# Kernel tuning notes

Measured on AMD Instinct MI355X. Metric: run time of the kernel, lower is better.

Reference implementation:

```python
import jax, jax.numpy as jnp
import numpy as np

NUM_ANGLE = 100
NUM_RHO = 100
EPS = 1e-5


def _dht_rho_indices(h, w, num_angle, num_rho):
    # Per the deep-hough-transform CUDA host code:
    # irho = (floor(sqrt(H^2+W^2)) + 1) / (numRho - 1); theta_k = k*pi/numAngle
    irho = (int(np.sqrt(h * h + w * w)) + 1) / float(num_rho - 1)
    theta = np.arange(num_angle) * (np.pi / num_angle)
    cos_t = np.cos(theta) / irho  # [A]
    sin_t = np.sin(theta) / irho
    yy = (np.arange(h) - h // 2).astype(np.float64)  # centered row coord
    xx = (np.arange(w) - w // 2).astype(np.float64)  # centered col coord
    # r[a, i, j] = round(xx*cos + yy*sin) + numRho//2
    r = np.round(xx[None, None, :] * cos_t[:, None, None]
                 + yy[None, :, None] * sin_t[:, None, None]).astype(np.int32)
    r = np.clip(r + num_rho // 2, 0, num_rho - 1)
    return jnp.asarray(r.reshape(num_angle, h * w))  # [A, HW]


def dht(feat, num_angle, num_rho):
    # Hough voting: scatter-add every pixel into one rho bin per angle.
    n, c, h, w = feat.shape
    idx = _dht_rho_indices(h, w, num_angle, num_rho)      # [A, HW] int32
    flat = feat.reshape(n * c, h * w).T                   # [HW, NC]
    seg = lambda ids: jax.ops.segment_sum(flat, ids, num_segments=num_rho)
    acc = jax.vmap(seg)(idx)                              # [A, R, NC]
    return acc.transpose(2, 0, 1).reshape(n, c, num_angle, num_rho)


def conv2d(x, wgt, b, pad):
    y = jax.lax.conv_general_dilated(
        x, wgt, window_strides=(1, 1), padding=[(pad, pad), (pad, pad)],
        dimension_numbers=("NCHW", "OIHW", "NCHW"))
    return y + b[None, :, None, None]


def bn_relu(x, gamma, beta):
    # BatchNorm in eval mode with running_mean=0, running_var=1.
    scale = gamma / np.sqrt(1.0 + EPS)
    return jax.nn.relu(x * scale[None, :, None, None] + beta[None, :, None, None])


def setup_inputs() -> dict:
    key = jax.random.key(0)
    ks = jax.random.split(key, 4)
    N, CIN, DIM, H, W = 16, 256, 128, 100, 100
    x = jax.random.normal(ks[0], (N, CIN, H, W), dtype=jnp.float32)
    w1 = jax.random.normal(ks[1], (DIM, CIN, 1, 1), dtype=jnp.float32) * 0.05
    w2 = jax.random.normal(ks[2], (DIM, DIM, 3, 3), dtype=jnp.float32) * 0.05
    w3 = jax.random.normal(ks[3], (DIM, DIM, 3, 3), dtype=jnp.float32) * 0.05
    zeros = jnp.zeros((DIM,), jnp.float32)
    ones = jnp.ones((DIM,), jnp.float32)
    return {
        "x": x,
        "w1": w1, "b1": zeros, "g1": ones, "be1": zeros,
        "w2": w2, "b2": zeros, "g2": ones, "be2": zeros,
        "w3": w3, "b3": zeros, "g3": ones, "be3": zeros,
    }


def reference(x, w1, b1, g1, be1, w2, b2, g2, be2, w3, b3, g3, be3):
    h = bn_relu(conv2d(x, w1, b1, 0), g1, be1)        # 1x1 conv + BN + ReLU
    h = dht(h, NUM_ANGLE, NUM_RHO)                    # Hough voting -> [N,C,A,R]
    h = bn_relu(conv2d(h, w2, b2, 1), g2, be2)        # 3x3 conv + BN + ReLU
    h = bn_relu(conv2d(h, w3, b3, 1), g3, be3)        # 3x3 conv + BN + ReLU
    return h
```

## Files before the change

### kernel.cpp

```cpp
#include <hip/hip_runtime.h>
#include <hip/hip_bf16.h>
#include <math.h>

#ifndef M_PI
#define M_PI 3.14159265358979323846
#endif

typedef unsigned short u16;
typedef short short8 __attribute__((ext_vector_type(8)));
typedef float f32x4 __attribute__((ext_vector_type(4)));
typedef float f32x2 __attribute__((ext_vector_type(2)));

#define CIN  256
#define CH   128
#define HW   10000
#define NA   100
#define NR   100

__device__ __forceinline__ float bf2f(u16 v) {
  return __uint_as_float(((unsigned int)v) << 16);
}
__device__ __forceinline__ u16 f2bf(float f) {
  unsigned int u = __float_as_uint(f);
  u += 0x7fffu + ((u >> 16) & 1u);
  return (u16)(u >> 16);
}
__device__ __forceinline__ f32x2 bfpair(unsigned int v) {
  f32x2 r;
  r.x = __uint_as_float(v << 16);
  r.y = __uint_as_float(v & 0xffff0000u);
  return r;
}

__global__ void __launch_bounds__(256)
k_prep_csr(const float* __restrict__ w1, const float* __restrict__ w2,
           const float* __restrict__ w3, u16* __restrict__ wbf1,
           u16* __restrict__ wbf2, u16* __restrict__ wbf3,
           u16* __restrict__ list, int* __restrict__ coff,
           int* __restrict__ woff) {
#pragma clang fp contract(off)
  __shared__ unsigned char sidx[HW];
  __shared__ unsigned short rowcnt[100][100];
  __shared__ int off[NR + 1];
  __shared__ int wstart[17];
  int b = blockIdx.x;
  int t = threadIdx.x;

  if (b >= 100) {
    int tt = (b - 100) * 256 + t;
    if (tt < 32768) {
      int j = tt & 7, lp = (tt >> 3) & 63, nf = (tt >> 9) & 7, kc = tt >> 12;
      int co = nf * 16 + (lp & 15);
      int ci = kc * 32 + (lp >> 4) * 8 + j;
      wbf1[tt] = f2bf(w1[co * CIN + ci]);
    }
    {
      int j = tt & 7, lp = (tt >> 3) & 63, nf = (tt >> 9) & 7, kc = (tt >> 12) & 3, tap = tt >> 14;
      int co = nf * 16 + (lp & 15);
      int ci = kc * 32 + (lp >> 4) * 8 + j;
      wbf2[tt] = f2bf(w2[(co * CH + ci) * 9 + tap]);
      wbf3[tt] = f2bf(w3[(co * CH + ci) * 9 + tap]);
    }
    return;
  }

  int a = b;
  double theta = (double)a * (M_PI / 100.0);
  double irho  = 142.0 / 99.0;
  double ct = cos(theta) / irho;
  double st = sin(theta) / irho;

  if (t < 100) {
    for (int q = 0; q < 50; ++q) ((unsigned int*)&rowcnt[t][0])[q] = 0;
    int base = t * 100;
    for (int j = 0; j < 100; ++j) {
      double s = (double)(j - 50) * ct + (double)(t - 50) * st;
      int r = (int)rint(s) + 50;
      r = r < 0 ? 0 : (r > 99 ? 99 : r);
      sidx[base + j] = (unsigned char)r;
      rowcnt[t][r]++;
    }
  }
  if (t < 17) wstart[t] = NR;
  __syncthreads();

  if (t < 100) {
    int running = 0;
    for (int cc = 0; cc < 100; ++cc) {
      int tmp = rowcnt[cc][t];
      rowcnt[cc][t] = (unsigned short)running;
      running += tmp;
    }
    off[t + 1] = running;
  }
  __syncthreads();

  if (t == 0) {
    off[0] = 0;
    for (int bb = 0; bb < NR; ++bb) {
      int cb = off[bb + 1];
      off[bb + 1] = off[bb] + cb;
    }
  }
  __syncthreads();
  if (t <= NR) coff[a * (NR + 1) + t] = off[t];

  if (t < NR) {
    int o0 = off[t], o1 = off[t + 1];
    int ow = (o0 + ((o1 - o0) >> 1)) * 16 / HW;
    ow = ow > 15 ? 15 : ow;
    atomicMin(&wstart[ow], t);
  }
  __syncthreads();
  if (t == 0) {
    wstart[16] = NR;
    for (int ww = 15; ww >= 0; --ww)
      if (wstart[ww] == NR) wstart[ww] = wstart[ww + 1];
  }
  __syncthreads();
  if (t < 17) woff[a * 20 + t] = wstart[t];

  if (t < 100) {
    u16* dst = list + (size_t)a * HW;
    int base = t * 100;
    for (int j = 0; j < 100; ++j) {
      int r = sidx[base + j];
      int pos = off[r] + rowcnt[t][r];
      rowcnt[t][r]++;
      dst[pos] = (u16)(base + j);
    }
  }
}

__global__ void __launch_bounds__(256)
k_xt(const float* __restrict__ x, u16* __restrict__ xt) {
  __shared__ u16 tl[64][70];
  int n = blockIdx.z, c0 = blockIdx.y * 64, h0 = blockIdx.x * 64;
  int t = threadIdx.x;
#pragma unroll
  for (int p = 0; p < 16; ++p) {
    int row = p * 4 + (t >> 6);
    int col = t & 63;
    int hw  = h0 + col;
    float v = (hw < HW) ? x[((size_t)n * CIN + c0 + row) * HW + hw] : 0.f;
    tl[row][col] = f2bf(v);
  }
  __syncthreads();
  int hr = t >> 2;
  int sc = (t & 3) * 16;
  int hw = h0 + hr;
  if (hw < HW) {
    u16 vals[16];
#pragma unroll
    for (int j = 0; j < 16; ++j) vals[j] = tl[sc + j][hr];
    u16* dst = xt + ((size_t)n * HW + hw) * CIN + c0 + sc;
    *(uint4*)(dst)     = *(uint4*)&vals[0];
    *(uint4*)(dst + 8) = *(uint4*)&vals[8];
  }
}

__global__ void __launch_bounds__(512)
k_conv1(const u16* __restrict__ xt, const u16* __restrict__ wbf1,
        const float* __restrict__ pb, const float* __restrict__ pg,
        const float* __restrict__ pbe, u16* __restrict__ h1t) {
  __shared__ uint4 lds4[4096];
  char* lds = (char*)lds4;
  int n  = blockIdx.y;
  int m0 = blockIdx.x * 128;
  int t  = threadIdx.x;
  int l  = t & 63, w = t >> 6, wm = w >> 2, wn = w & 3;

  {
    int r16 = t >> 5;
    int seg = t & 31;
#pragma unroll
    for (int p = 0; p < 8; ++p) {
      int m  = p * 16 + r16;
      int hw = m0 + m;
      uint4 v = make_uint4(0, 0, 0, 0);
      if (hw < HW) v = *(const uint4*)(xt + ((size_t)n * HW + hw) * CIN + seg * 8);
      *(uint4*)(lds + m * 512 + ((seg * 16) ^ ((m & 31) << 4))) = v;
    }
  }
  __syncthreads();

  int kseg = (l >> 4) * 16;
  f32x4 acc[4][2];
  f32x4 zf = {0.f, 0.f, 0.f, 0.f};
#pragma unroll
  for (int i = 0; i < 4; ++i)
#pragma unroll
    for (int j = 0; j < 2; ++j) acc[i][j] = zf;

  for (int kc = 0; kc < 8; ++kc) {
    short8 afr[4], bfr[2];
#pragma unroll
    for (int fm = 0; fm < 4; ++fm) {
      int m = wm * 64 + fm * 16 + (l & 15);
      afr[fm] = *(const short8*)(lds + m * 512 + ((kc * 64 + kseg) ^ ((m & 31) << 4)));
    }
#pragma unroll
    for (int fn = 0; fn < 2; ++fn)
      bfr[fn] = *(const short8*)(wbf1 + (((size_t)kc * 8 + wn * 2 + fn) * 64 + l) * 8);
#pragma unroll
    for (int fm = 0; fm < 4; ++fm)
#pragma unroll
      for (int fn = 0; fn < 2; ++fn)
        acc[fm][fn] = __builtin_amdgcn_mfma_f32_16x16x32_bf16(afr[fm], bfr[fn], acc[fm][fn], 0, 0, 0);
  }

  float sc[2], sh[2];
#pragma unroll
  for (int fn = 0; fn < 2; ++fn) {
    int co = wn * 32 + fn * 16 + (l & 15);
    float s = pg[co] / sqrtf(1.f + 1e-5f);
    sc[fn] = s;
    sh[fn] = pb[co] * s + pbe[co];
  }

  __syncthreads();
#pragma unroll
  for (int fm = 0; fm < 4; ++fm)
#pragma unroll
    for (int fn = 0; fn < 2; ++fn) {
      int co = wn * 32 + fn * 16 + (l & 15);
#pragma unroll
      for (int q = 0; q < 4; ++q) {
        int m = wm * 64 + fm * 16 + (l >> 4) * 4 + q;
        float y = fmaxf(acc[fm][fn][q] * sc[fn] + sh[fn], 0.f);
        *(u16*)(lds + m * 256 + ((co * 2) ^ ((m & 15) << 4))) = f2bf(y);
      }
    }
  __syncthreads();
#pragma unroll
  for (int p = 0; p < 4; ++p) {
    int e = p * 512 + t;
    int m = e >> 4;
    int hw = m0 + m;
    if (hw < HW) {
      uint4 v = *(const uint4*)(lds + m * 256 + (((e & 15) * 16) ^ ((m & 15) << 4)));
      *(uint4*)(h1t + ((size_t)n * HW + hw) * CH + (e & 15) * 8) = v;
    }
  }
}

__global__ void __launch_bounds__(256)
k_dht(const u16* __restrict__ h1t, const u16* __restrict__ list,
      const int* __restrict__ coff, const int* __restrict__ woff,
      u16* __restrict__ dht) {
  int id  = blockIdx.x;
  int x   = id & 7;
  int rem = id >> 3;
  int hi  = rem >= 400;
  int n   = (x << 1) | hi;
  int aq  = hi ? rem - 400 : rem;
  int a   = aq >> 2;
  int q   = aq & 3;
  int t   = threadIdx.x;
  int c   = t & 63;
  int w   = (t >> 6) + q * 4;

  const char* nimg = (const char*)h1t + (size_t)n * HW * 256;
  const int  c4    = c * 4;
  const u16* lst   = list + (size_t)a * HW;
  const int* cof   = coff + a * (NR + 1);
  const int* wof   = woff + a * 20;
  unsigned int* out32 = (unsigned int*)(dht + ((size_t)(n * NA + a) * NR) * CH) + c;

  int rlo = __builtin_amdgcn_readfirstlane(wof[w]);
  int rhi = __builtin_amdgcn_readfirstlane(wof[w + 1]);
  if (rlo >= rhi) return;

  int o0 = __builtin_amdgcn_readfirstlane(cof[rlo]);
  for (int r = rlo; r < rhi; ++r) {
    int o1 = __builtin_amdgcn_readfirstlane(cof[r + 1]);

    f32x2 A0 = {0.f, 0.f}, A1 = {0.f, 0.f};
    int k = o0;

    if (k & 1) {
      int p = __builtin_amdgcn_readfirstlane((int)lst[k]);
      unsigned int v = *(const unsigned int*)((nimg + ((size_t)p << 8)) + c4);
      A0 += bfpair(v);
      ++k;
    }

    for (; k + 16 <= o1; k += 16) {
      unsigned int ids[8];
#pragma unroll
      for (int j = 0; j < 8; ++j)
        ids[j] = __builtin_amdgcn_readfirstlane(*(const unsigned int*)(lst + k + 2 * j));
      unsigned int v[16];
#pragma unroll
      for (int j = 0; j < 8; ++j) {
        int p0 = (int)(ids[j] & 0xffffu);
        int p1 = (int)(ids[j] >> 16);
        v[2 * j]     = *(const unsigned int*)((nimg + ((size_t)p0 << 8)) + c4);
        v[2 * j + 1] = *(const unsigned int*)((nimg + ((size_t)p1 << 8)) + c4);
      }
#pragma unroll
      for (int j = 0; j < 16; ++j) {
        if (j & 1) A1 += bfpair(v[j]);
        else       A0 += bfpair(v[j]);
      }
    }
    for (; k + 2 <= o1; k += 2) {
      unsigned int ids = __builtin_amdgcn_readfirstlane(*(const unsigned int*)(lst + k));
      int p0 = (int)(ids & 0xffffu);
      int p1 = (int)(ids >> 16);
      unsigned int v0 = *(const unsigned int*)((nimg + ((size_t)p0 << 8)) + c4);
      unsigned int v1 = *(const unsigned int*)((nimg + ((size_t)p1 << 8)) + c4);
      A0 += bfpair(v0);
      A1 += bfpair(v1);
    }
    if (k < o1) {
      int p = __builtin_amdgcn_readfirstlane((int)lst[k]);
      unsigned int v = *(const unsigned int*)((nimg + ((size_t)p << 8)) + c4);
      A0 += bfpair(v);
    }

    float ax = A0.x + A1.x;
    float ay = A0.y + A1.y;
    unsigned int pk = (unsigned int)f2bf(ax) | ((unsigned int)f2bf(ay) << 16);
    out32[(size_t)r << 6] = pk;
    o0 = o1;
  }
}

template <int OUT_MODE>
__global__ void __launch_bounds__(512)
k_conv3x3(const u16* __restrict__ X, const u16* __restrict__ wbf,
          const float* __restrict__ pb, const float* __restrict__ pg,
          const float* __restrict__ pbe, void* __restrict__ out) {
  __shared__ uint4 lds4[2880];
  char* lds = (char*)lds4;
  int n    = blockIdx.y;
  int tile = blockIdx.x;
  int ta = tile / 13, tr = tile - ta * 13;
  int a0 = ta * 16, r0 = tr * 8;
  int t  = threadIdx.x;
  int l  = t & 63, w = t >> 6, wm = w >> 2, wn = w & 3;

  {
    int sr32 = t >> 4;
    int cb   = (t & 15) * 16;
#pragma unroll
    for (int p = 0; p < 6; ++p) {
      int s = p * 32 + sr32;
      if (s < 180) {
        int sa = a0 - 1 + s / 10;
        int sr = r0 - 1 + s % 10;
        uint4 v = make_uint4(0, 0, 0, 0);
        if (sa >= 0 && sa < NA && sr >= 0 && sr < NR)
          v = *(const uint4*)(X + ((size_t)(n * NA + sa) * NR + sr) * CH + (t & 15) * 8);
        *(uint4*)(lds + s * 256 + (cb ^ ((s & 15) << 4))) = v;
      }
    }
  }
  __syncthreads();

  int sbase[4];
#pragma unroll
  for (int fm = 0; fm < 4; ++fm) {
    int m = wm * 64 + fm * 16 + (l & 15);
    sbase[fm] = ((m >> 3) + 1) * 10 + (m & 7) + 1;
  }
  int kseg = (l >> 4) * 16;

  f32x4 acc[4][2];
  f32x4 zf = {0.f, 0.f, 0.f, 0.f};
#pragma unroll
  for (int i = 0; i < 4; ++i)
#pragma unroll
    for (int j = 0; j < 2; ++j) acc[i][j] = zf;

  for (int tap = 0; tap < 9; ++tap) {
    int soff = (tap / 3 - 1) * 10 + (tap % 3 - 1);
#pragma unroll
    for (int kc = 0; kc < 4; ++kc) {
      short8 afr[4], bfr[2];
#pragma unroll
      for (int fm = 0; fm < 4; ++fm) {
        int s = sbase[fm] + soff;
        afr[fm] = *(const short8*)(lds + s * 256 + ((kc * 64 + kseg) ^ ((s & 15) << 4)));
      }
#pragma unroll
      for (int fn = 0; fn < 2; ++fn)
        bfr[fn] = *(const short8*)(wbf + (((size_t)(tap * 4 + kc) * 8 + wn * 2 + fn) * 64 + l) * 8);
#pragma unroll
      for (int fm = 0; fm < 4; ++fm)
#pragma unroll
        for (int fn = 0; fn < 2; ++fn)
          acc[fm][fn] = __builtin_amdgcn_mfma_f32_16x16x32_bf16(afr[fm], bfr[fn], acc[fm][fn], 0, 0, 0);
    }
  }

  float sc[2], sh[2];
#pragma unroll
  for (int fn = 0; fn < 2; ++fn) {
    int co = wn * 32 + fn * 16 + (l & 15);
    float s = pg[co] / sqrtf(1.f + 1e-5f);
    sc[fn] = s;
    sh[fn] = pb[co] * s + pbe[co];
  }

  if (OUT_MODE == 0) {
    __syncthreads();
#pragma unroll
    for (int fm = 0; fm < 4; ++fm)
#pragma unroll
      for (int fn = 0; fn < 2; ++fn) {
        int co = wn * 32 + fn * 16 + (l & 15);
#pragma unroll
        for (int q = 0; q < 4; ++q) {
          int m = wm * 64 + fm * 16 + (l >> 4) * 4 + q;
          float y = fmaxf(acc[fm][fn][q] * sc[fn] + sh[fn], 0.f);
          *(u16*)(lds + m * 256 + ((co * 2) ^ ((m & 15) << 4))) = f2bf(y);
        }
      }
    __syncthreads();
    u16* o = (u16*)out;
#pragma unroll
    for (int p = 0; p < 4; ++p) {
      int e = p * 512 + t;
      int m = e >> 4;
      int a = a0 + (m >> 3), r = r0 + (m & 7);
      if (a < NA && r < NR) {
        uint4 v = *(const uint4*)(lds + m * 256 + (((e & 15) * 16) ^ ((m & 15) << 4)));
        *(uint4*)(o + ((size_t)(n * NA + a) * NR + r) * CH + (e & 15) * 8) = v;
      }
    }
  } else {
    float* o = (float*)out;
#pragma unroll
    for (int fm = 0; fm < 4; ++fm) {
      int mb = wm * 64 + fm * 16 + (l >> 4) * 4;
      int a  = a0 + (mb >> 3), rr = r0 + (mb & 7);
      if (a < NA && rr < NR) {
#pragma unroll
        for (int fn = 0; fn < 2; ++fn) {
          int co = wn * 32 + fn * 16 + (l & 15);
          float4 v;
          v.x = fmaxf(acc[fm][fn][0] * sc[fn] + sh[fn], 0.f);
          v.y = fmaxf(acc[fm][fn][1] * sc[fn] + sh[fn], 0.f);
          v.z = fmaxf(acc[fm][fn][2] * sc[fn] + sh[fn], 0.f);
          v.w = fmaxf(acc[fm][fn][3] * sc[fn] + sh[fn], 0.f);
          *(float4*)(o + ((size_t)n * CH + co) * HW + a * NR + rr) = v;
        }
      }
    }
  }
}

extern "C" void kernel_launch(void* const* d_in, const int* in_sizes, int n_in,
                              void* d_out, int out_size, void* d_ws, size_t ws_size,
                              hipStream_t stream) {
  if (n_in < 13) return;
  const float* x   = (const float*)d_in[0];
  const float* w1  = (const float*)d_in[1];
  const float* b1  = (const float*)d_in[2];
  const float* g1  = (const float*)d_in[3];
  const float* be1 = (const float*)d_in[4];
  const float* w2  = (const float*)d_in[5];
  const float* b2  = (const float*)d_in[6];
  const float* g2  = (const float*)d_in[7];
  const float* be2 = (const float*)d_in[8];
  const float* w3  = (const float*)d_in[9];
  const float* b3  = (const float*)d_in[10];
  const float* g3  = (const float*)d_in[11];
  const float* be3 = (const float*)d_in[12];

  const size_t o_list = 0;
  const size_t o_coff = 2000128;
  const size_t o_woff = 2040576;
  const size_t o_wbf1 = 2048768;
  const size_t o_wbf2 = o_wbf1 + 65536;
  const size_t o_wbf3 = o_wbf2 + 294912;
  const size_t o_dht  = o_wbf3 + 294912;
  const size_t o_c2   = o_dht + 40960000;
  const size_t need   = o_dht + 81920000;
  if (ws_size < need) return;

  char*  ws   = (char*)d_ws;
  u16*   list = (u16*)(ws + o_list);
  int*   coff = (int*)(ws + o_coff);
  int*   woff = (int*)(ws + o_woff);
  u16*   wbf1 = (u16*)(ws + o_wbf1);
  u16*   wbf2 = (u16*)(ws + o_wbf2);
  u16*   wbf3 = (u16*)(ws + o_wbf3);
  u16*   xt   = (u16*)(ws + o_dht);
  u16*   dht  = (u16*)(ws + o_dht);
  u16*   c2   = (u16*)(ws + o_c2);
  u16*   h1t  = (u16*)d_out;

  k_prep_csr<<<dim3(676), dim3(256), 0, stream>>>(w1, w2, w3, wbf1, wbf2, wbf3, list, coff, woff);
  k_xt<<<dim3(157, 4, 16), dim3(256), 0, stream>>>(x, xt);
  k_conv1<<<dim3(79, 16), dim3(512), 0, stream>>>(xt, wbf1, b1, g1, be1, h1t);
  k_dht<<<dim3(6400), dim3(256), 0, stream>>>(h1t, list, coff, woff, dht);
  k_conv3x3<0><<<dim3(91, 16), dim3(512), 0, stream>>>(dht, wbf2, b2, g2, be2, (void*)c2);
  k_conv3x3<1><<<dim3(91, 16), dim3(512), 0, stream>>>(c2, wbf3, b3, g3, be3, d_out);
}
```

Before: 415.5 us.

## Switch 3x3 conv MFMA from 16x16x32 to 32x32x16 with new warp tiling

Rewrites the 3x3 conv inner loop to use 32x32x16 bf16 MFMA instructions, with each wave covering 32 rows by 64 output channels instead of 64 by 32. The conv2/conv3 weight pre-pack layout is changed to match the new B-fragment layout, and both epilogues are remapped to the 32x32 accumulator register layout. The aim is fewer MFMA issues and fewer LDS A-fragment reads per FLOP. In exchange, B-fragment global loads per wave double relative to A reuse.

```diff
diff --git a/kernel.cpp b/kernel.cpp
--- a/kernel.cpp
+++ b/kernel.cpp
@@ -10,6 +10,7 @@
 typedef short short8 __attribute__((ext_vector_type(8)));
 typedef float f32x4 __attribute__((ext_vector_type(4)));
 typedef float f32x2 __attribute__((ext_vector_type(2)));
+typedef float f32x16 __attribute__((ext_vector_type(16)));
 
 #define CIN  256
 #define CH   128
@@ -55,9 +56,13 @@
       wbf1[tt] = f2bf(w1[co * CIN + ci]);
     }
     {
-      int j = tt & 7, lp = (tt >> 3) & 63, nf = (tt >> 9) & 7, kc = (tt >> 12) & 3, tap = tt >> 14;
-      int co = nf * 16 + (lp & 15);
-      int ci = kc * 32 + (lp >> 4) * 8 + j;
+      int j   = tt & 7;
+      int lp  = (tt >> 3) & 63;
+      int nf  = (tt >> 9) & 3;
+      int k16 = (tt >> 11) & 7;
+      int tap = tt >> 14;
+      int co  = nf * 32 + (lp & 31);
+      int ci  = k16 * 16 + (lp >> 5) * 8 + j;
       wbf2[tt] = f2bf(w2[(co * CH + ci) * 9 + tap]);
       wbf3[tt] = f2bf(w3[(co * CH + ci) * 9 + tap]);
     }
@@ -339,7 +344,7 @@
   int ta = tile / 13, tr = tile - ta * 13;
   int a0 = ta * 16, r0 = tr * 8;
   int t  = threadIdx.x;
-  int l  = t & 63, w = t >> 6, wm = w >> 2, wn = w & 3;
+  int l  = t & 63, w = t >> 6, wm = w >> 1, wn = w & 1;
 
   {
     int sr32 = t >> 4;
@@ -359,46 +364,37 @@
   }
   __syncthreads();
 
-  int sbase[4];
-#pragma unroll
-  for (int fm = 0; fm < 4; ++fm) {
-    int m = wm * 64 + fm * 16 + (l & 15);
-    sbase[fm] = ((m >> 3) + 1) * 10 + (m & 7) + 1;
-  }
-  int kseg = (l >> 4) * 16;
-
-  f32x4 acc[4][2];
-  f32x4 zf = {0.f, 0.f, 0.f, 0.f};
-#pragma unroll
-  for (int i = 0; i < 4; ++i)
-#pragma unroll
-    for (int j = 0; j < 2; ++j) acc[i][j] = zf;
+  int mrow  = wm * 32 + (l & 31);
+  int sbase = ((mrow >> 3) + 1) * 10 + (mrow & 7) + 1;
+  int kcol  = (l >> 5) * 16;
+
+  f32x16 acc[2];
+#pragma unroll
+  for (int i = 0; i < 2; ++i)
+#pragma unroll
+    for (int q = 0; q < 16; ++q) acc[i][q] = 0.f;
 
   for (int tap = 0; tap < 9; ++tap) {
     int soff = (tap / 3 - 1) * 10 + (tap % 3 - 1);
-#pragma unroll
-    for (int kc = 0; kc < 4; ++kc) {
-      short8 afr[4], bfr[2];
-#pragma unroll
-      for (int fm = 0; fm < 4; ++fm) {
-        int s = sbase[fm] + soff;
-        afr[fm] = *(const short8*)(lds + s * 256 + ((kc * 64 + kseg) ^ ((s & 15) << 4)));
-      }
+    int s = sbase + soff;
+    int sw = (s & 15) << 4;
+#pragma unroll
+    for (int k16 = 0; k16 < 8; ++k16) {
+      short8 afr = *(const short8*)(lds + s * 256 + ((k16 * 32 + kcol) ^ sw));
+      short8 bfr[2];
 #pragma unroll
       for (int fn = 0; fn < 2; ++fn)
-        bfr[fn] = *(const short8*)(wbf + (((size_t)(tap * 4 + kc) * 8 + wn * 2 + fn) * 64 + l) * 8);
-#pragma unroll
-      for (int fm = 0; fm < 4; ++fm)
-#pragma unroll
-        for (int fn = 0; fn < 2; ++fn)
-          acc[fm][fn] = __builtin_amdgcn_mfma_f32_16x16x32_bf16(afr[fm], bfr[fn], acc[fm][fn], 0, 0, 0);
+        bfr[fn] = *(const short8*)(wbf + (((size_t)(tap * 8 + k16) * 4 + wn * 2 + fn) * 64 + l) * 8);
+#pragma unroll
+      for (int fn = 0; fn < 2; ++fn)
+        acc[fn] = __builtin_amdgcn_mfma_f32_32x32x16_bf16(afr, bfr[fn], acc[fn], 0, 0, 0);
     }
   }
 
   float sc[2], sh[2];
 #pragma unroll
   for (int fn = 0; fn < 2; ++fn) {
-    int co = wn * 32 + fn * 16 + (l & 15);
+    int co = wn * 64 + fn * 32 + (l & 31);
     float s = pg[co] / sqrtf(1.f + 1e-5f);
     sc[fn] = s;
     sh[fn] = pb[co] * s + pbe[co];
@@ -407,17 +403,15 @@
   if (OUT_MODE == 0) {
     __syncthreads();
 #pragma unroll
-    for (int fm = 0; fm < 4; ++fm)
-#pragma unroll
-      for (int fn = 0; fn < 2; ++fn) {
-        int co = wn * 32 + fn * 16 + (l & 15);
-#pragma unroll
-        for (int q = 0; q < 4; ++q) {
-          int m = wm * 64 + fm * 16 + (l >> 4) * 4 + q;
-          float y = fmaxf(acc[fm][fn][q] * sc[fn] + sh[fn], 0.f);
-          *(u16*)(lds + m * 256 + ((co * 2) ^ ((m & 15) << 4))) = f2bf(y);
-        }
-      }
+    for (int fn = 0; fn < 2; ++fn) {
+      int co = wn * 64 + fn * 32 + (l & 31);
+#pragma unroll
+      for (int reg = 0; reg < 16; ++reg) {
+        int m = wm * 32 + (reg & 3) + 8 * (reg >> 2) + 4 * (l >> 5);
+        float y = fmaxf(acc[fn][reg] * sc[fn] + sh[fn], 0.f);
+        *(u16*)(lds + m * 256 + ((co * 2) ^ ((m & 15) << 4))) = f2bf(y);
+      }
+    }
     __syncthreads();
     u16* o = (u16*)out;
 #pragma unroll
@@ -433,18 +427,18 @@
   } else {
     float* o = (float*)out;
 #pragma unroll
-    for (int fm = 0; fm < 4; ++fm) {
-      int mb = wm * 64 + fm * 16 + (l >> 4) * 4;
-      int a  = a0 + (mb >> 3), rr = r0 + (mb & 7);
-      if (a < NA && rr < NR) {
-#pragma unroll
-        for (int fn = 0; fn < 2; ++fn) {
-          int co = wn * 32 + fn * 16 + (l & 15);
+    for (int fn = 0; fn < 2; ++fn) {
+      int co = wn * 64 + fn * 32 + (l & 31);
+#pragma unroll
+      for (int q = 0; q < 4; ++q) {
+        int mb = wm * 32 + 8 * q + 4 * (l >> 5);
+        int a  = a0 + (mb >> 3), rr = r0 + (mb & 7);
+        if (a < NA && rr < NR) {
           float4 v;
-          v.x = fmaxf(acc[fm][fn][0] * sc[fn] + sh[fn], 0.f);
-          v.y = fmaxf(acc[fm][fn][1] * sc[fn] + sh[fn], 0.f);
-          v.z = fmaxf(acc[fm][fn][2] * sc[fn] + sh[fn], 0.f);
-          v.w = fmaxf(acc[fm][fn][3] * sc[fn] + sh[fn], 0.f);
+          v.x = fmaxf(acc[fn][4 * q + 0] * sc[fn] + sh[fn], 0.f);
+          v.y = fmaxf(acc[fn][4 * q + 1] * sc[fn] + sh[fn], 0.f);
+          v.z = fmaxf(acc[fn][4 * q + 2] * sc[fn] + sh[fn], 0.f);
+          v.w = fmaxf(acc[fn][4 * q + 3] * sc[fn] + sh[fn], 0.f);
           *(float4*)(o + ((size_t)n * CH + co) * HW + a * NR + rr) = v;
         }
       }
```

New measurement: 446.7 us. 1.08x slower.

## Fuse input transpose into 1x1 conv and fold BN scale into weights

Applied to the files above, without the earlier changes.

Removes the separate transpose/bf16-cast kernel. The 1x1 conv now reads fp32 NCHW input directly and converts it to bf16 in registers, with weights as the A operand and pixels as the B operand. The BN scale is folded into the bf16 weights during prep, and a precomputed bias vector replaces the per-thread scale/shift math. This saves one full write and read of the transposed activation, but the input loads are now strided per channel (8 separate loads per fragment) rather than vectorized 16-byte loads.

```diff
diff --git a/kernel.cpp b/kernel.cpp
--- a/kernel.cpp
+++ b/kernel.cpp
@@ -34,8 +34,10 @@
 
 __global__ void __launch_bounds__(256)
 k_prep_csr(const float* __restrict__ w1, const float* __restrict__ w2,
-           const float* __restrict__ w3, u16* __restrict__ wbf1,
-           u16* __restrict__ wbf2, u16* __restrict__ wbf3,
+           const float* __restrict__ w3, const float* __restrict__ g1,
+           const float* __restrict__ b1, const float* __restrict__ be1,
+           u16* __restrict__ wbf1, u16* __restrict__ wbf2,
+           u16* __restrict__ wbf3, float* __restrict__ bias1,
            u16* __restrict__ list, int* __restrict__ coff,
            int* __restrict__ woff) {
 #pragma clang fp contract(off)
@@ -52,7 +54,12 @@
       int j = tt & 7, lp = (tt >> 3) & 63, nf = (tt >> 9) & 7, kc = tt >> 12;
       int co = nf * 16 + (lp & 15);
       int ci = kc * 32 + (lp >> 4) * 8 + j;
-      wbf1[tt] = f2bf(w1[co * CIN + ci]);
+      float s = g1[co] / sqrtf(1.f + 1e-5f);
+      wbf1[tt] = f2bf(w1[co * CIN + ci] * s);
+    }
+    if (b == 100 && t < 128) {
+      float s = g1[t] / sqrtf(1.f + 1e-5f);
+      bias1[t] = b1[t] * s + be1[t];
     }
     {
       int j = tt & 7, lp = (tt >> 3) & 63, nf = (tt >> 9) & 7, kc = (tt >> 12) & 3, tap = tt >> 14;
@@ -132,59 +139,19 @@
   }
 }
 
-__global__ void __launch_bounds__(256)
-k_xt(const float* __restrict__ x, u16* __restrict__ xt) {
-  __shared__ u16 tl[64][70];
-  int n = blockIdx.z, c0 = blockIdx.y * 64, h0 = blockIdx.x * 64;
-  int t = threadIdx.x;
-#pragma unroll
-  for (int p = 0; p < 16; ++p) {
-    int row = p * 4 + (t >> 6);
-    int col = t & 63;
-    int hw  = h0 + col;
-    float v = (hw < HW) ? x[((size_t)n * CIN + c0 + row) * HW + hw] : 0.f;
-    tl[row][col] = f2bf(v);
-  }
-  __syncthreads();
-  int hr = t >> 2;
-  int sc = (t & 3) * 16;
-  int hw = h0 + hr;
-  if (hw < HW) {
-    u16 vals[16];
-#pragma unroll
-    for (int j = 0; j < 16; ++j) vals[j] = tl[sc + j][hr];
-    u16* dst = xt + ((size_t)n * HW + hw) * CIN + c0 + sc;
-    *(uint4*)(dst)     = *(uint4*)&vals[0];
-    *(uint4*)(dst + 8) = *(uint4*)&vals[8];
-  }
-}
-
 __global__ void __launch_bounds__(512)
-k_conv1(const u16* __restrict__ xt, const u16* __restrict__ wbf1,
-        const float* __restrict__ pb, const float* __restrict__ pg,
-        const float* __restrict__ pbe, u16* __restrict__ h1t) {
-  __shared__ uint4 lds4[4096];
-  char* lds = (char*)lds4;
-  int n  = blockIdx.y;
-  int m0 = blockIdx.x * 128;
-  int t  = threadIdx.x;
-  int l  = t & 63, w = t >> 6, wm = w >> 2, wn = w & 3;
-
-  {
-    int r16 = t >> 5;
-    int seg = t & 31;
-#pragma unroll
-    for (int p = 0; p < 8; ++p) {
-      int m  = p * 16 + r16;
-      int hw = m0 + m;
-      uint4 v = make_uint4(0, 0, 0, 0);
-      if (hw < HW) v = *(const uint4*)(xt + ((size_t)n * HW + hw) * CIN + seg * 8);
-      *(uint4*)(lds + m * 512 + ((seg * 16) ^ ((m & 31) << 4))) = v;
-    }
-  }
-  __syncthreads();
-
-  int kseg = (l >> 4) * 16;
+k_conv1(const float* __restrict__ x, const u16* __restrict__ wbf1,
+        const float* __restrict__ bias1, u16* __restrict__ h1t) {
+  __shared__ char lds[32768];
+  int n   = blockIdx.y;
+  int hw0 = blockIdx.x * 128;
+  int t   = threadIdx.x;
+  int l   = t & 63, w = t >> 6, wm = w >> 2, wn = w & 3;
+
+  const float* xn = x + (size_t)n * CIN * HW;
+  int hwb  = hw0 + wn * 32 + (l & 15);
+  int cinb = (l >> 4) * 8;
+
   f32x4 acc[4][2];
   f32x4 zf = {0.f, 0.f, 0.f, 0.f};
 #pragma unroll
@@ -193,15 +160,25 @@
     for (int j = 0; j < 2; ++j) acc[i][j] = zf;
 
   for (int kc = 0; kc < 8; ++kc) {
-    short8 afr[4], bfr[2];
-#pragma unroll
-    for (int fm = 0; fm < 4; ++fm) {
-      int m = wm * 64 + fm * 16 + (l & 15);
-      afr[fm] = *(const short8*)(lds + m * 512 + ((kc * 64 + kseg) ^ ((m & 31) << 4)));
-    }
-#pragma unroll
-    for (int fn = 0; fn < 2; ++fn)
-      bfr[fn] = *(const short8*)(wbf1 + (((size_t)kc * 8 + wn * 2 + fn) * 64 + l) * 8);
+    short8 afr[4];
+#pragma unroll
+    for (int fm = 0; fm < 4; ++fm)
+      afr[fm] = *(const short8*)(wbf1 + (((size_t)kc * 8 + wm * 4 + fm) * 64 + l) * 8);
+    short8 bfr[2];
+#pragma unroll
+    for (int fn = 0; fn < 2; ++fn) {
+      int hw = hwb + fn * 16;
+      const float* col = xn + (size_t)(kc * 32 + cinb) * HW + hw;
+      u16 vals[8];
+      if (hw < HW) {
+#pragma unroll
+        for (int j = 0; j < 8; ++j) vals[j] = f2bf(col[(size_t)j * HW]);
+      } else {
+#pragma unroll
+        for (int j = 0; j < 8; ++j) vals[j] = 0;
+      }
+      bfr[fn] = *(const short8*)vals;
+    }
 #pragma unroll
     for (int fm = 0; fm < 4; ++fm)
 #pragma unroll
@@ -209,26 +186,23 @@
         acc[fm][fn] = __builtin_amdgcn_mfma_f32_16x16x32_bf16(afr[fm], bfr[fn], acc[fm][fn], 0, 0, 0);
   }
 
-  float sc[2], sh[2];
-#pragma unroll
-  for (int fn = 0; fn < 2; ++fn) {
-    int co = wn * 32 + fn * 16 + (l & 15);
-    float s = pg[co] / sqrtf(1.f + 1e-5f);
-    sc[fn] = s;
-    sh[fn] = pb[co] * s + pbe[co];
-  }
-
-  __syncthreads();
+  float bi[4][4];
 #pragma unroll
   for (int fm = 0; fm < 4; ++fm)
 #pragma unroll
+    for (int q = 0; q < 4; ++q)
+      bi[fm][q] = bias1[wm * 64 + fm * 16 + (l >> 4) * 4 + q];
+
+#pragma unroll
+  for (int fm = 0; fm < 4; ++fm)
+#pragma unroll
     for (int fn = 0; fn < 2; ++fn) {
-      int co = wn * 32 + fn * 16 + (l & 15);
+      int mrow = wn * 32 + fn * 16 + (l & 15);
 #pragma unroll
       for (int q = 0; q < 4; ++q) {
-        int m = wm * 64 + fm * 16 + (l >> 4) * 4 + q;
-        float y = fmaxf(acc[fm][fn][q] * sc[fn] + sh[fn], 0.f);
-        *(u16*)(lds + m * 256 + ((co * 2) ^ ((m & 15) << 4))) = f2bf(y);
+        int co = wm * 64 + fm * 16 + (l >> 4) * 4 + q;
+        float y = fmaxf(acc[fm][fn][q] + bi[fm][q], 0.f);
+        *(u16*)(lds + mrow * 256 + ((co * 2) ^ ((mrow & 15) << 4))) = f2bf(y);
       }
     }
   __syncthreads();
@@ -236,7 +210,7 @@
   for (int p = 0; p < 4; ++p) {
     int e = p * 512 + t;
     int m = e >> 4;
-    int hw = m0 + m;
+    int hw = hw0 + m;
     if (hw < HW) {
       uint4 v = *(const uint4*)(lds + m * 256 + (((e & 15) * 16) ^ ((m & 15) << 4)));
       *(uint4*)(h1t + ((size_t)n * HW + hw) * CH + (e & 15) * 8) = v;
@@ -470,32 +444,34 @@
   const float* g3  = (const float*)d_in[11];
   const float* be3 = (const float*)d_in[12];
 
-  const size_t o_list = 0;
-  const size_t o_coff = 2000128;
-  const size_t o_woff = 2040576;
-  const size_t o_wbf1 = 2048768;
-  const size_t o_wbf2 = o_wbf1 + 65536;
-  const size_t o_wbf3 = o_wbf2 + 294912;
-  const size_t o_dht  = o_wbf3 + 294912;
-  const size_t o_c2   = o_dht + 40960000;
-  const size_t need   = o_dht + 81920000;
+  const size_t o_list  = 0;
+  const size_t o_coff  = 2000128;
+  const size_t o_woff  = 2040576;
+  const size_t o_wbf1  = 2048768;
+  const size_t o_wbf2  = o_wbf1 + 65536;
+  const size_t o_wbf3  = o_wbf2 + 294912;
+  const size_t o_bias1 = o_wbf3 + 294912;
+  const size_t o_dht   = o_bias1 + 1024;
+  const size_t o_c2    = o_dht + 40960000;
+  const size_t need    = o_c2 + 40960000;
   if (ws_size < need) return;
 
-  char*  ws   = (char*)d_ws;
-  u16*   list = (u16*)(ws + o_list);
-  int*   coff = (int*)(ws + o_coff);
-  int*   woff = (int*)(ws + o_woff);
-  u16*   wbf1 = (u16*)(ws + o_wbf1);
-  u16*   wbf2 = (u16*)(ws + o_wbf2);
-  u16*   wbf3 = (u16*)(ws + o_wbf3);
-  u16*   xt   = (u16*)(ws + o_dht);
-  u16*   dht  = (u16*)(ws + o_dht);
-  u16*   c2   = (u16*)(ws + o_c2);
-  u16*   h1t  = (u16*)d_out;
-
-  k_prep_csr<<<dim3(676), dim3(256), 0, stream>>>(w1, w2, w3, wbf1, wbf2, wbf3, list, coff, woff);
-  k_xt<<<dim3(157, 4, 16), dim3(256), 0, stream>>>(x, xt);
-  k_conv1<<<dim3(79, 16), dim3(512), 0, stream>>>(xt, wbf1, b1, g1, be1, h1t);
+  char*  ws    = (char*)d_ws;
+  u16*   list  = (u16*)(ws + o_list);
+  int*   coff  = (int*)(ws + o_coff);
+  int*   woff  = (int*)(ws + o_woff);
+  u16*   wbf1  = (u16*)(ws + o_wbf1);
+  u16*   wbf2  = (u16*)(ws + o_wbf2);
+  u16*   wbf3  = (u16*)(ws + o_wbf3);
+  float* bias1 = (float*)(ws + o_bias1);
+  u16*   dht   = (u16*)(ws + o_dht);
+  u16*   c2    = (u16*)(ws + o_c2);
+  u16*   h1t   = (u16*)d_out;
+
+  k_prep_csr<<<dim3(676), dim3(256), 0, stream>>>(w1, w2, w3, g1, b1, be1,
+                                                  wbf1, wbf2, wbf3, bias1,
+                                                  list, coff, woff);
+  k_conv1<<<dim3(79, 16), dim3(512), 0, stream>>>(x, wbf1, bias1, h1t);
   k_dht<<<dim3(6400), dim3(256), 0, stream>>>(h1t, list, coff, woff, dht);
   k_conv3x3<0><<<dim3(91, 16), dim3(512), 0, stream>>>(dht, wbf2, b2, g2, be2, (void*)c2);
   k_conv3x3<1><<<dim3(91, 16), dim3(512), 0, stream>>>(c2, wbf3, b3, g3, be3, d_out);
```

After: 391.7 us, median of 2. 5.7% less time.
